# Kernel optimization log

Measured on AMD Instinct MI355X. Metric: run time of the kernel, lower is better.

Reference implementation:

```python
import jax, jax.numpy as jnp
import numpy as np
from jax import lax

D = 1024
N_EXP = 8
DD = 4 * D
BS = 8192
TRAIN_CAP = 1.0
LN_EPS = 1e-5


def setup_inputs() -> dict:
    key = jax.random.key(0)
    ks = jax.random.split(key, 8)
    s = 0.02
    return {
        "x": jax.random.normal(ks[0], (BS, D), jnp.float32),
        "Wg": jax.random.normal(ks[1], (N_EXP, D), jnp.float32) * s,
        "cp_w1": jax.random.normal(ks[2], (D, D), jnp.float32) * s,
        "cp_b1": jnp.zeros((D,), jnp.float32),
        "cp_w2": jax.random.normal(ks[3], (N_EXP, D), jnp.float32) * s,
        "cp_b2": jnp.zeros((N_EXP,), jnp.float32),
        "ln_g": jnp.ones((D,), jnp.float32),
        "ln_b": jnp.zeros((D,), jnp.float32),
        "fc1s": jax.random.normal(ks[4], (N_EXP, DD, D), jnp.float32) * s,
        "b1s": jnp.zeros((N_EXP, DD), jnp.float32),
        "fc2s": jax.random.normal(ks[5], (N_EXP, D, DD), jnp.float32) * s,
        "b2s": jnp.zeros((N_EXP, D), jnp.float32),
    }


def reference(x, Wg, cp_w1, cp_b1, cp_w2, cp_b2, ln_g, ln_b, fc1s, b1s, fc2s, b2s):
    bs, d = x.shape
    n = Wg.shape[0]
    k = int(bs * TRAIN_CAP) // n  # tokens kept per expert

    # gate scores in (0,1): (tanh(x Wg^T)+1)/2   -> [bs, n]
    scores = (jnp.tanh(x @ Wg.T) + 1.0) * 0.5

    # per-expert descending sort of tokens by score
    order = jnp.argsort(-scores, axis=0)                      # [bs, n]
    sorted_w = jnp.take_along_axis(scores, order, axis=0)     # [bs, n]
    kept_w = sorted_w[:k]                                     # [k, n]
    kept_idx = order[:k]                                      # [k, n]

    # keep mask (labels for capacity predictor)
    keep_mask = jnp.zeros((bs, n), x.dtype).at[kept_idx, jnp.arange(n)[None, :]].set(1.0)

    # capacity predictor loss (BCE with logits, x detached)
    xd = lax.stop_gradient(x)
    h = jax.nn.gelu(xd @ cp_w1.T + cp_b1, approximate=True)
    logits = h @ cp_w2.T + cp_b2                              # [bs, n]
    cap_loss = jnp.mean(jnp.logaddexp(0.0, logits) - logits * keep_mask)

    # dispatch: gather selected tokens, row-major flatten of [k, n]
    idx = kept_idx.reshape(-1)                                # [k*n]
    y = x[idx]                                                # [k*n, d]

    # LayerNorm
    mu = y.mean(-1, keepdims=True)
    var = y.var(-1, keepdims=True)
    y = (y - mu) * lax.rsqrt(var + LN_EPS) * ln_g + ln_b

    # per-expert grouped GEMMs
    y3 = y.reshape(k, n, d)
    h1 = jnp.einsum('knd,nfd->knf', y3, fc1s) + b1s[None]     # [k, n, dd]
    h1 = jax.nn.gelu(h1, approximate=True)
    y2 = jnp.einsum('knf,ndf->knd', h1, fc2s) + b2s[None]     # [k, n, d]

    # weight by gate score and scatter-add back (residual)
    y2 = y2 * kept_w[..., None]
    out = x.at[idx].add(y2.reshape(k * n, d))
    return out, cap_loss
```

## Files before the change

kernel.cpp:

```cpp
#include <hip/hip_runtime.h>


#define BS_   8192
#define D_    1024
#define DD_   4096
#define NEXP  8
#define KCAP  1024

typedef unsigned int   uint32;
typedef unsigned short u16;
typedef __bf16 bf16x8  __attribute__((ext_vector_type(8)));
typedef float  f32x4   __attribute__((ext_vector_type(4)));
typedef u16    u16x8   __attribute__((ext_vector_type(8)));
typedef u16    u16x4   __attribute__((ext_vector_type(4)));

__device__ __forceinline__ u16 f2bf(float f){
  uint32 u = __float_as_uint(f);
  u = (u + 0x7fffu + ((u >> 16) & 1u)) >> 16;
  return (u16)u;
}
__device__ __forceinline__ float bf_lo(uint32 u){ return __uint_as_float(u << 16); }
__device__ __forceinline__ float bf_hi(uint32 u){ return __uint_as_float(u & 0xffff0000u); }

__device__ __forceinline__ float gelu_fast(float v){
  const float u2 = v * (1.5957691216057308f + 0.07135481282962162f * v * v);
  const float e  = __expf(u2);
  return v - v / (1.0f + e);
}
__device__ __forceinline__ void glds16(const u16* g, u16* l){
  __builtin_amdgcn_global_load_lds(
      (const __attribute__((address_space(1))) unsigned int*)g,
      (__attribute__((address_space(3))) unsigned int*)l, 16, 0, 0);
}

__global__ __launch_bounds__(256)
void convert_kernel(const float* __restrict__ in, u16* __restrict__ out, int n)
{
  const int stride = gridDim.x * 256 * 8;
  for (int idx = (blockIdx.x * 256 + threadIdx.x) * 8; idx < n; idx += stride){
    const float4 a = *(const float4*)(in + idx);
    const float4 b = *(const float4*)(in + idx + 4);
    u16x8 o;
    o[0]=f2bf(a.x); o[1]=f2bf(a.y); o[2]=f2bf(a.z); o[3]=f2bf(a.w);
    o[4]=f2bf(b.x); o[5]=f2bf(b.y); o[6]=f2bf(b.z); o[7]=f2bf(b.w);
    *(u16x8*)(out + idx) = o;
  }
}

__global__ __launch_bounds__(64)
void gating_kernel(const float* __restrict__ x, const float* __restrict__ Wg,
                   float* __restrict__ scores, uint32* __restrict__ keep_bits,
                   u16* __restrict__ xh)
{
  const int i    = blockIdx.x;
  const int lane = threadIdx.x;
  const float* xr = x + (size_t)i * D_ + lane * 16;
  const float4 x0 = *(const float4*)(xr +  0);
  const float4 x1 = *(const float4*)(xr +  4);
  const float4 x2 = *(const float4*)(xr +  8);
  const float4 x3 = *(const float4*)(xr + 12);
  u16x8 p0, p1;
  p0[0]=f2bf(x0.x); p0[1]=f2bf(x0.y); p0[2]=f2bf(x0.z); p0[3]=f2bf(x0.w);
  p0[4]=f2bf(x1.x); p0[5]=f2bf(x1.y); p0[6]=f2bf(x1.z); p0[7]=f2bf(x1.w);
  p1[0]=f2bf(x2.x); p1[1]=f2bf(x2.y); p1[2]=f2bf(x2.z); p1[3]=f2bf(x2.w);
  p1[4]=f2bf(x3.x); p1[5]=f2bf(x3.y); p1[6]=f2bf(x3.z); p1[7]=f2bf(x3.w);
  *(u16x8*)(xh + (size_t)i * D_ + lane * 16)     = p0;
  *(u16x8*)(xh + (size_t)i * D_ + lane * 16 + 8) = p1;

  float acc[NEXP];
  #pragma unroll
  for (int e = 0; e < NEXP; e++){
    const float* wr = Wg + e * D_ + lane * 16;
    const float4 w0 = *(const float4*)(wr +  0);
    const float4 w1 = *(const float4*)(wr +  4);
    const float4 w2 = *(const float4*)(wr +  8);
    const float4 w3 = *(const float4*)(wr + 12);
    float s = x0.x*w0.x + x0.y*w0.y + x0.z*w0.z + x0.w*w0.w;
    s += x1.x*w1.x + x1.y*w1.y + x1.z*w1.z + x1.w*w1.w;
    s += x2.x*w2.x + x2.y*w2.y + x2.z*w2.z + x2.w*w2.w;
    s += x3.x*w3.x + x3.y*w3.y + x3.z*w3.z + x3.w*w3.w;
    acc[e] = s;
  }
  #pragma unroll
  for (int e = 0; e < NEXP; e++){
    #pragma unroll
    for (int off = 32; off >= 1; off >>= 1) acc[e] += __shfl_xor(acc[e], off);
  }
  if (lane == 0){
    #pragma unroll
    for (int e = 0; e < NEXP; e++) scores[i * NEXP + e] = (tanhf(acc[e]) + 1.0f) * 0.5f;
    keep_bits[i] = 0u;
  }
}

__global__ __launch_bounds__(256)
void select_kernel(const float* __restrict__ scores, uint32* __restrict__ keep_bits,
                   int* __restrict__ counts, int* __restrict__ rowlist,
                   float* __restrict__ wlist, int* __restrict__ inv)
{
  __shared__ unsigned long long sk[2048];
  const int e = blockIdx.y;
  const int i = blockIdx.x * 256 + threadIdx.x;
  const float ms = scores[i * NEXP + e];
  const unsigned long long mk =
      ((unsigned long long)__float_as_uint(ms) << 32) | (uint32)(BS_ - 1 - i);
  int cnt = 0;
  for (int base = 0; base < BS_; base += 2048){
    #pragma unroll
    for (int u = 0; u < 8; u++){
      const int j = base + (int)threadIdx.x * 8 + u;
      const float sj = scores[j * NEXP + e];
      sk[threadIdx.x * 8 + u] =
          ((unsigned long long)__float_as_uint(sj) << 32) | (uint32)(BS_ - 1 - j);
    }
    __syncthreads();
    #pragma unroll 8
    for (int jj = 0; jj < 2048; jj++) cnt += (sk[jj] > mk) ? 1 : 0;
    __syncthreads();
  }
  if (cnt < KCAP){
    const int slot = atomicAdd(&counts[e], 1);
    rowlist[e * KCAP + slot] = i;
    wlist[e * KCAP + slot]   = ms;
    inv[i * NEXP + e]        = slot;
    atomicOr(&keep_bits[i], 1u << e);
  }
}

template<bool GELU_EP, bool OUT_BF16>
__global__ __launch_bounds__(256)
void gemm_bt16(const u16* __restrict__ A, const u16* __restrict__ B,
               const float* __restrict__ bias, void* __restrict__ Cv,
               int M, int N, int K,
               long long sA, long long sB, long long sBias, long long sC)
{
  __shared__ u16 smA[128 * 32];
  __shared__ u16 smB[128 * 32];
  const int z    = blockIdx.z;
  const int m0   = blockIdx.y * 128;
  const int n0   = blockIdx.x * 128;
  const int tid  = threadIdx.x;
  const int lane = tid & 63, wv = tid >> 6;
  const int l15  = lane & 15, quad = lane >> 4;
  const int moff = (wv >> 1) * 64, noff = (wv & 1) * 64;

  const int srow = wv * 32 + (lane >> 2);
  const int skol = (lane & 3) * 8;
  const u16* Ag = A + (long long)z * sA + (long long)(m0 + srow) * K + skol;
  const u16* Bg = B + (long long)z * sB + (long long)(n0 + srow) * K + skol;
  u16* lA = smA + wv * 1024;
  u16* lB = smB + wv * 1024;

  f32x4 acc[4][4];
  #pragma unroll
  for (int i = 0; i < 4; i++)
    #pragma unroll
    for (int j = 0; j < 4; j++)
      acc[i][j] = (f32x4){0.f, 0.f, 0.f, 0.f};

  for (int k0 = 0; k0 < K; k0 += 32){
    #pragma unroll
    for (int c = 0; c < 2; c++){
      glds16(Ag + (long long)(c * 16) * K + k0, lA + c * 512);
      glds16(Bg + (long long)(c * 16) * K + k0, lB + c * 512);
    }
    __syncthreads();
    bf16x8 aF[4], bF[4];
    #pragma unroll
    for (int i = 0; i < 4; i++)
      aF[i] = *(const bf16x8*)(smA + (moff + i * 16 + l15) * 32 + quad * 8);
    #pragma unroll
    for (int j = 0; j < 4; j++)
      bF[j] = *(const bf16x8*)(smB + (noff + j * 16 + l15) * 32 + quad * 8);
    #pragma unroll
    for (int i = 0; i < 4; i++)
      #pragma unroll
      for (int j = 0; j < 4; j++)
        acc[i][j] = __builtin_amdgcn_mfma_f32_16x16x32_bf16(bF[j], aF[i], acc[i][j], 0, 0, 0);
    __syncthreads();
  }

  const float* biasp = bias + (long long)z * sBias;
  const long long cbase = (long long)z * sC;
  #pragma unroll
  for (int i = 0; i < 4; i++){
    const int gm = m0 + moff + i * 16 + l15;
    const long long rowb = cbase + (long long)gm * N;
    #pragma unroll
    for (int j = 0; j < 4; j++){
      const int gn = n0 + noff + j * 16 + quad * 4;
      const float4 bv = *(const float4*)(biasp + gn);
      float v0 = acc[i][j][0] + bv.x;
      float v1 = acc[i][j][1] + bv.y;
      float v2 = acc[i][j][2] + bv.z;
      float v3 = acc[i][j][3] + bv.w;
      if constexpr (GELU_EP){
        v0 = gelu_fast(v0); v1 = gelu_fast(v1);
        v2 = gelu_fast(v2); v3 = gelu_fast(v3);
      }
      if constexpr (OUT_BF16){
        u16x4 o; o[0]=f2bf(v0); o[1]=f2bf(v1); o[2]=f2bf(v2); o[3]=f2bf(v3);
        *(u16x4*)((u16*)Cv + rowb + gn) = o;
      } else {
        *(float4*)((float*)Cv + rowb + gn) = make_float4(v0, v1, v2, v3);
      }
    }
  }
}

__global__ __launch_bounds__(256)
void loss_kernel(const u16* __restrict__ h, const float* __restrict__ cp_w2,
                 const float* __restrict__ cp_b2, const uint32* __restrict__ keep_bits,
                 float* __restrict__ loss)
{
  __shared__ float bl;
  if (threadIdx.x == 0) bl = 0.f;
  __syncthreads();
  const int wv = threadIdx.x >> 6, lane = threadIdx.x & 63;
  const int i  = blockIdx.x * 4 + wv;
  const u16* hr = h + (size_t)i * D_ + lane * 16;
  const uint4 ha = *(const uint4*)(hr);
  const uint4 hb = *(const uint4*)(hr + 8);
  float hx[16];
  hx[0]=bf_lo(ha.x); hx[1]=bf_hi(ha.x); hx[2]=bf_lo(ha.y); hx[3]=bf_hi(ha.y);
  hx[4]=bf_lo(ha.z); hx[5]=bf_hi(ha.z); hx[6]=bf_lo(ha.w); hx[7]=bf_hi(ha.w);
  hx[8]=bf_lo(hb.x); hx[9]=bf_hi(hb.x); hx[10]=bf_lo(hb.y); hx[11]=bf_hi(hb.y);
  hx[12]=bf_lo(hb.z); hx[13]=bf_hi(hb.z); hx[14]=bf_lo(hb.w); hx[15]=bf_hi(hb.w);
  float acc[NEXP];
  #pragma unroll
  for (int e = 0; e < NEXP; e++){
    const float* wr = cp_w2 + e * D_ + lane * 16;
    const float4 w0 = *(const float4*)(wr +  0);
    const float4 w1 = *(const float4*)(wr +  4);
    const float4 w2 = *(const float4*)(wr +  8);
    const float4 w3 = *(const float4*)(wr + 12);
    float s = hx[0]*w0.x + hx[1]*w0.y + hx[2]*w0.z + hx[3]*w0.w;
    s += hx[4]*w1.x + hx[5]*w1.y + hx[6]*w1.z + hx[7]*w1.w;
    s += hx[8]*w2.x + hx[9]*w2.y + hx[10]*w2.z + hx[11]*w2.w;
    s += hx[12]*w3.x + hx[13]*w3.y + hx[14]*w3.z + hx[15]*w3.w;
    acc[e] = s;
  }
  #pragma unroll
  for (int e = 0; e < NEXP; e++){
    #pragma unroll
    for (int off = 32; off >= 1; off >>= 1) acc[e] += __shfl_xor(acc[e], off);
  }
  if (lane == 0){
    const uint32 kb = keep_bits[i];
    float li = 0.f;
    #pragma unroll
    for (int e = 0; e < NEXP; e++){
      const float l  = acc[e] + cp_b2[e];
      const float sp = fmaxf(l, 0.f) + log1pf(expf(-fabsf(l)));
      li += sp - l * (float)((kb >> e) & 1u);
    }
    atomicAdd(&bl, li);
  }
  __syncthreads();
  if (threadIdx.x == 0) atomicAdd(loss, bl);
}

__global__ __launch_bounds__(256)
void ln_gather_kernel(const float* __restrict__ x, const int* __restrict__ rowlist,
                      const float* __restrict__ ln_g, const float* __restrict__ ln_b,
                      u16* __restrict__ Y)
{
  __shared__ float red[8];
  const int b   = blockIdx.x;
  const int row = rowlist[b];
  const int tid = threadIdx.x;
  const float4 v = *(const float4*)(x + (size_t)row * D_ + tid * 4);
  float s = v.x + v.y + v.z + v.w;
  float q = v.x*v.x + v.y*v.y + v.z*v.z + v.w*v.w;
  const int lane = tid & 63, wv = tid >> 6;
  #pragma unroll
  for (int off = 32; off >= 1; off >>= 1){ s += __shfl_xor(s, off); q += __shfl_xor(q, off); }
  if (lane == 0){ red[wv] = s; red[4 + wv] = q; }
  __syncthreads();
  s = red[0] + red[1] + red[2] + red[3];
  q = red[4] + red[5] + red[6] + red[7];
  const float mu  = s * (1.0f / D_);
  const float var = q * (1.0f / D_) - mu * mu;
  const float rs  = rsqrtf(var + 1e-5f);
  const float4 g  = *(const float4*)(ln_g + tid * 4);
  const float4 bb = *(const float4*)(ln_b + tid * 4);
  u16x4 o;
  o[0] = f2bf((v.x - mu) * rs * g.x + bb.x);
  o[1] = f2bf((v.y - mu) * rs * g.y + bb.y);
  o[2] = f2bf((v.z - mu) * rs * g.z + bb.z);
  o[3] = f2bf((v.w - mu) * rs * g.w + bb.w);
  *(u16x4*)(&Y[(size_t)b * D_ + tid * 4]) = o;
}

__global__ __launch_bounds__(256)
void combine_kernel(const float* __restrict__ x, const uint32* __restrict__ keep_bits,
                    const int* __restrict__ inv, const float* __restrict__ wlist,
                    const float* __restrict__ Y2, float* __restrict__ out)
{
  const int i = blockIdx.x;
  const int c = threadIdx.x * 4;
  float4 v = *(const float4*)(x + (size_t)i * D_ + c);
  uint32 kb = keep_bits[i];
  while (kb){
    const int e = __ffs(kb) - 1;
    kb &= kb - 1;
    const int r = inv[i * NEXP + e];
    const float w = wlist[e * KCAP + r];
    const float4 y = *(const float4*)(Y2 + ((size_t)(e * KCAP + r)) * D_ + c);
    v.x += w * y.x; v.y += w * y.y; v.z += w * y.z; v.w += w * y.w;
  }
  *(float4*)(out + (size_t)i * D_ + c) = v;
}

__global__ void finalize_loss_kernel(const float* __restrict__ loss, float* __restrict__ outp){
  outp[0] = loss[0] * (1.0f / (float)(BS_ * NEXP));
}

extern "C" void kernel_launch(void* const* d_in, const int* in_sizes, int n_in,
                              void* d_out, int out_size, void* d_ws, size_t ws_size,
                              hipStream_t stream)
{
  const float* x     = (const float*)d_in[0];
  const float* Wg    = (const float*)d_in[1];
  const float* cp_w1 = (const float*)d_in[2];
  const float* cp_b1 = (const float*)d_in[3];
  const float* cp_w2 = (const float*)d_in[4];
  const float* cp_b2 = (const float*)d_in[5];
  const float* ln_g  = (const float*)d_in[6];
  const float* ln_b  = (const float*)d_in[7];
  const float* fc1s  = (const float*)d_in[8];
  const float* b1s   = (const float*)d_in[9];
  const float* fc2s  = (const float*)d_in[10];
  const float* b2s   = (const float*)d_in[11];
  float* out = (float*)d_out;

  char* p = (char*)d_ws;
  auto take = [&](size_t bytes) -> char* {
    char* r = p; p += (bytes + 255) & ~(size_t)255; return r;
  };
  float*  scores    = (float*) take((size_t)BS_ * NEXP * 4);
  int*    counts    = (int*)   take(256);
  float*  loss      = (float*) take(256);
  int*    rowlist   = (int*)   take((size_t)BS_ * 4);
  float*  wlist     = (float*) take((size_t)BS_ * 4);
  uint32* keep_bits = (uint32*)take((size_t)BS_ * 4);
  int*    inv       = (int*)   take((size_t)BS_ * NEXP * 4);
  u16*    xh        = (u16*)   take((size_t)BS_ * D_ * 2);
  u16*    cpw1h     = (u16*)   take((size_t)D_ * D_ * 2);
  u16*    fc1h      = (u16*)   take((size_t)NEXP * DD_ * D_ * 2);
  u16*    fc2h      = (u16*)   take((size_t)NEXP * D_ * DD_ * 2);
  u16*    H1        = (u16*)   take((size_t)NEXP * KCAP * DD_ * 2);
  u16*    h_cp      = (u16*)   take((size_t)BS_ * D_ * 2);
  u16*    Y         = (u16*)   take((size_t)NEXP * KCAP * D_ * 2);
  float*  Y2        = (float*)h_cp;

  hipMemsetAsync(counts, 0, 512, stream);

  convert_kernel<<<512,  256, 0, stream>>>(cp_w1, cpw1h, D_ * D_);
  convert_kernel<<<8192, 256, 0, stream>>>(fc1s, fc1h, NEXP * DD_ * D_);
  convert_kernel<<<8192, 256, 0, stream>>>(fc2s, fc2h, NEXP * D_ * DD_);

  gating_kernel<<<BS_, 64, 0, stream>>>(x, Wg, scores, keep_bits, xh);

  select_kernel<<<dim3(BS_ / 256, NEXP), 256, 0, stream>>>(
      scores, keep_bits, counts, rowlist, wlist, inv);

  gemm_bt16<true, true><<<dim3(D_ / 128, BS_ / 128, 1), 256, 0, stream>>>(
      xh, cpw1h, cp_b1, h_cp, BS_, D_, D_, 0, 0, 0, 0);

  loss_kernel<<<BS_ / 4, 256, 0, stream>>>(h_cp, cp_w2, cp_b2, keep_bits, loss);

  ln_gather_kernel<<<BS_, 256, 0, stream>>>(x, rowlist, ln_g, ln_b, Y);

  gemm_bt16<true, true><<<dim3(DD_ / 128, KCAP / 128, NEXP), 256, 0, stream>>>(
      Y, fc1h, b1s, H1, KCAP, DD_, D_,
      (long long)KCAP * D_, (long long)DD_ * D_, DD_, (long long)KCAP * DD_);

  gemm_bt16<false, false><<<dim3(D_ / 128, KCAP / 128, NEXP), 256, 0, stream>>>(
      H1, fc2h, b2s, Y2, KCAP, D_, DD_,
      (long long)KCAP * DD_, (long long)D_ * DD_, D_, (long long)KCAP * D_);

  combine_kernel<<<BS_, 256, 0, stream>>>(x, keep_bits, inv, wlist, Y2, out);

  finalize_loss_kernel<<<1, 1, 0, stream>>>(loss, out + (size_t)BS_ * D_);
}
```

Before: 881.4 us.

## Pre-pack B weights into MFMA fragment order, load B from registers, split-K fc2

Weight conversion now writes the B operands in MFMA fragment order, so each lane loads its bf16x8 B fragment straight from global memory into registers, prefetched one K step ahead, instead of staging B through shared memory. This halves LDS traffic and footprint per block. The fc2 GEMM is also split two ways along K into two fp32 partial buffers, which doubles the grid. Bias is added in the combine kernel while it sums the partials. The cost is more global traffic for the partials and a B fragment layout that depends on K being a multiple of 32.

```diff
diff --git a/kernel.cpp b/kernel.cpp
--- a/kernel.cpp
+++ b/kernel.cpp
@@ -34,17 +34,22 @@
 }
 
 __global__ __launch_bounds__(256)
-void convert_kernel(const float* __restrict__ in, u16* __restrict__ out, int n)
-{
-  const int stride = gridDim.x * 256 * 8;
-  for (int idx = (blockIdx.x * 256 + threadIdx.x) * 8; idx < n; idx += stride){
-    const float4 a = *(const float4*)(in + idx);
-    const float4 b = *(const float4*)(in + idx + 4);
-    u16x8 o;
-    o[0]=f2bf(a.x); o[1]=f2bf(a.y); o[2]=f2bf(a.z); o[3]=f2bf(a.w);
-    o[4]=f2bf(b.x); o[5]=f2bf(b.y); o[6]=f2bf(b.z); o[7]=f2bf(b.w);
-    *(u16x8*)(out + idx) = o;
-  }
+void pack_b_kernel(const float* __restrict__ in, u16* __restrict__ out,
+                   int K, int kshift)
+{
+  const long long t = (long long)blockIdx.x * 256 + threadIdx.x;
+  const int  lane  = (int)(t & 63);
+  const long long brick = t >> 6;
+  const long long n16 = brick >> kshift;
+  const int  k32  = (int)(brick & ((1 << kshift) - 1));
+  const float* src = in + (n16 * 16 + (lane & 15)) * (long long)K
+                        + k32 * 32 + (lane >> 4) * 8;
+  const float4 a = *(const float4*)src;
+  const float4 b = *(const float4*)(src + 4);
+  u16x8 o;
+  o[0]=f2bf(a.x); o[1]=f2bf(a.y); o[2]=f2bf(a.z); o[3]=f2bf(a.w);
+  o[4]=f2bf(b.x); o[5]=f2bf(b.y); o[6]=f2bf(b.z); o[7]=f2bf(b.w);
+  *(u16x8*)(out + t * 8) = o;
 }
 
 __global__ __launch_bounds__(64)
@@ -127,16 +132,19 @@
   }
 }
 
-template<bool GELU_EP, bool OUT_BF16>
-__global__ __launch_bounds__(256)
-void gemm_bt16(const u16* __restrict__ A, const u16* __restrict__ B,
-               const float* __restrict__ bias, void* __restrict__ Cv,
-               int M, int N, int K,
-               long long sA, long long sB, long long sBias, long long sC)
+template<bool GELU_EP, bool OUT_BF16, int SPLIT>
+__global__ __launch_bounds__(256)
+void gemm_pk(const u16* __restrict__ A, const u16* __restrict__ Bp,
+             const float* __restrict__ bias, void* __restrict__ Cv,
+             float* __restrict__ P0, float* __restrict__ P1,
+             int M, int N, int K,
+             long long sA, long long sBp, long long sBias, long long sC)
 {
   __shared__ u16 smA[128 * 32];
-  __shared__ u16 smB[128 * 32];
-  const int z    = blockIdx.z;
+  const int zr   = blockIdx.z;
+  const int z    = zr / SPLIT, ks = zr % SPLIT;
+  const int kb0  = (K / SPLIT) * ks;
+  const int kIt0 = kb0 >> 5, kIt1 = (kb0 + K / SPLIT) >> 5;
   const int m0   = blockIdx.y * 128;
   const int n0   = blockIdx.x * 128;
   const int tid  = threadIdx.x;
@@ -147,9 +155,12 @@
   const int srow = wv * 32 + (lane >> 2);
   const int skol = (lane & 3) * 8;
   const u16* Ag = A + (long long)z * sA + (long long)(m0 + srow) * K + skol;
-  const u16* Bg = B + (long long)z * sB + (long long)(n0 + srow) * K + skol;
   u16* lA = smA + wv * 1024;
-  u16* lB = smB + wv * 1024;
+
+  const int nk32 = K >> 5;
+  const long long jstr = (long long)nk32 * 512;
+  const u16* Bfrag = Bp + (long long)z * sBp
+                   + ((long long)((n0 + noff) >> 4)) * jstr + (long long)lane * 8;
 
   f32x4 acc[4][4];
   #pragma unroll
@@ -158,51 +169,74 @@
     for (int j = 0; j < 4; j++)
       acc[i][j] = (f32x4){0.f, 0.f, 0.f, 0.f};
 
-  for (int k0 = 0; k0 < K; k0 += 32){
-    #pragma unroll
-    for (int c = 0; c < 2; c++){
-      glds16(Ag + (long long)(c * 16) * K + k0, lA + c * 512);
-      glds16(Bg + (long long)(c * 16) * K + k0, lB + c * 512);
-    }
+  bf16x8 bF[4], bN[4];
+  #pragma unroll
+  for (int j = 0; j < 4; j++)
+    bF[j] = *(const bf16x8*)(Bfrag + j * jstr + (long long)kIt0 * 512);
+
+  for (int kk = kIt0; kk < kIt1; kk++){
+    glds16(Ag + kk * 32,           lA);
+    glds16(Ag + 16 * K + kk * 32,  lA + 512);
     __syncthreads();
-    bf16x8 aF[4], bF[4];
+    const bool more = (kk + 1 < kIt1);
+    if (more){
+      #pragma unroll
+      for (int j = 0; j < 4; j++)
+        bN[j] = *(const bf16x8*)(Bfrag + j * jstr + (long long)(kk + 1) * 512);
+    }
+    bf16x8 aF[4];
     #pragma unroll
     for (int i = 0; i < 4; i++)
       aF[i] = *(const bf16x8*)(smA + (moff + i * 16 + l15) * 32 + quad * 8);
-    #pragma unroll
-    for (int j = 0; j < 4; j++)
-      bF[j] = *(const bf16x8*)(smB + (noff + j * 16 + l15) * 32 + quad * 8);
     #pragma unroll
     for (int i = 0; i < 4; i++)
       #pragma unroll
       for (int j = 0; j < 4; j++)
         acc[i][j] = __builtin_amdgcn_mfma_f32_16x16x32_bf16(bF[j], aF[i], acc[i][j], 0, 0, 0);
     __syncthreads();
-  }
-
-  const float* biasp = bias + (long long)z * sBias;
-  const long long cbase = (long long)z * sC;
-  #pragma unroll
-  for (int i = 0; i < 4; i++){
-    const int gm = m0 + moff + i * 16 + l15;
-    const long long rowb = cbase + (long long)gm * N;
-    #pragma unroll
-    for (int j = 0; j < 4; j++){
-      const int gn = n0 + noff + j * 16 + quad * 4;
-      const float4 bv = *(const float4*)(biasp + gn);
-      float v0 = acc[i][j][0] + bv.x;
-      float v1 = acc[i][j][1] + bv.y;
-      float v2 = acc[i][j][2] + bv.z;
-      float v3 = acc[i][j][3] + bv.w;
-      if constexpr (GELU_EP){
-        v0 = gelu_fast(v0); v1 = gelu_fast(v1);
-        v2 = gelu_fast(v2); v3 = gelu_fast(v3);
+    if (more){
+      #pragma unroll
+      for (int j = 0; j < 4; j++) bF[j] = bN[j];
+    }
+  }
+
+  if constexpr (SPLIT > 1){
+    float* Pout = (ks == 0 ? P0 : P1) + (long long)z * sC;
+    #pragma unroll
+    for (int i = 0; i < 4; i++){
+      const int gm = m0 + moff + i * 16 + l15;
+      #pragma unroll
+      for (int j = 0; j < 4; j++){
+        const int gn = n0 + noff + j * 16 + quad * 4;
+        *(float4*)(Pout + (long long)gm * N + gn) =
+            make_float4(acc[i][j][0], acc[i][j][1], acc[i][j][2], acc[i][j][3]);
       }
-      if constexpr (OUT_BF16){
-        u16x4 o; o[0]=f2bf(v0); o[1]=f2bf(v1); o[2]=f2bf(v2); o[3]=f2bf(v3);
-        *(u16x4*)((u16*)Cv + rowb + gn) = o;
-      } else {
-        *(float4*)((float*)Cv + rowb + gn) = make_float4(v0, v1, v2, v3);
+    }
+  } else {
+    const float* biasp = bias + (long long)z * sBias;
+    const long long cbase = (long long)z * sC;
+    #pragma unroll
+    for (int i = 0; i < 4; i++){
+      const int gm = m0 + moff + i * 16 + l15;
+      const long long rowb = cbase + (long long)gm * N;
+      #pragma unroll
+      for (int j = 0; j < 4; j++){
+        const int gn = n0 + noff + j * 16 + quad * 4;
+        const float4 bv = *(const float4*)(biasp + gn);
+        float v0 = acc[i][j][0] + bv.x;
+        float v1 = acc[i][j][1] + bv.y;
+        float v2 = acc[i][j][2] + bv.z;
+        float v3 = acc[i][j][3] + bv.w;
+        if constexpr (GELU_EP){
+          v0 = gelu_fast(v0); v1 = gelu_fast(v1);
+          v2 = gelu_fast(v2); v3 = gelu_fast(v3);
+        }
+        if constexpr (OUT_BF16){
+          u16x4 o; o[0]=f2bf(v0); o[1]=f2bf(v1); o[2]=f2bf(v2); o[3]=f2bf(v3);
+          *(u16x4*)((u16*)Cv + rowb + gn) = o;
+        } else {
+          *(float4*)((float*)Cv + rowb + gn) = make_float4(v0, v1, v2, v3);
+        }
       }
     }
   }
@@ -295,7 +329,8 @@
 __global__ __launch_bounds__(256)
 void combine_kernel(const float* __restrict__ x, const uint32* __restrict__ keep_bits,
                     const int* __restrict__ inv, const float* __restrict__ wlist,
-                    const float* __restrict__ Y2, float* __restrict__ out)
+                    const float* __restrict__ P0, const float* __restrict__ P1,
+                    const float* __restrict__ b2s, float* __restrict__ out)
 {
   const int i = blockIdx.x;
   const int c = threadIdx.x * 4;
@@ -306,8 +341,14 @@
     kb &= kb - 1;
     const int r = inv[i * NEXP + e];
     const float w = wlist[e * KCAP + r];
-    const float4 y = *(const float4*)(Y2 + ((size_t)(e * KCAP + r)) * D_ + c);
-    v.x += w * y.x; v.y += w * y.y; v.z += w * y.z; v.w += w * y.w;
+    const size_t ro = ((size_t)(e * KCAP + r)) * D_ + c;
+    const float4 p0 = *(const float4*)(P0 + ro);
+    const float4 p1 = *(const float4*)(P1 + ro);
+    const float4 b2 = *(const float4*)(b2s + (size_t)e * D_ + c);
+    v.x += w * (p0.x + p1.x + b2.x);
+    v.y += w * (p0.y + p1.y + b2.y);
+    v.z += w * (p0.z + p1.z + b2.z);
+    v.w += w * (p0.w + p1.w + b2.w);
   }
   *(float4*)(out + (size_t)i * D_ + c) = v;
 }
@@ -346,41 +387,42 @@
   uint32* keep_bits = (uint32*)take((size_t)BS_ * 4);
   int*    inv       = (int*)   take((size_t)BS_ * NEXP * 4);
   u16*    xh        = (u16*)   take((size_t)BS_ * D_ * 2);
-  u16*    cpw1h     = (u16*)   take((size_t)D_ * D_ * 2);
-  u16*    fc1h      = (u16*)   take((size_t)NEXP * DD_ * D_ * 2);
-  u16*    fc2h      = (u16*)   take((size_t)NEXP * D_ * DD_ * 2);
+  u16*    cpw1p     = (u16*)   take((size_t)D_ * D_ * 2);
+  u16*    fc1p      = (u16*)   take((size_t)NEXP * DD_ * D_ * 2);
+  u16*    fc2p      = (u16*)   take((size_t)NEXP * D_ * DD_ * 2);
   u16*    H1        = (u16*)   take((size_t)NEXP * KCAP * DD_ * 2);
   u16*    h_cp      = (u16*)   take((size_t)BS_ * D_ * 2);
   u16*    Y         = (u16*)   take((size_t)NEXP * KCAP * D_ * 2);
-  float*  Y2        = (float*)h_cp;
+  float*  Pt0       = (float*)xh;
+  float*  Pt1       = (float*)((char*)xh + ((size_t)32 << 20));
 
   hipMemsetAsync(counts, 0, 512, stream);
 
-  convert_kernel<<<512,  256, 0, stream>>>(cp_w1, cpw1h, D_ * D_);
-  convert_kernel<<<8192, 256, 0, stream>>>(fc1s, fc1h, NEXP * DD_ * D_);
-  convert_kernel<<<8192, 256, 0, stream>>>(fc2s, fc2h, NEXP * D_ * DD_);
+  pack_b_kernel<<<(D_ * D_ / 8) / 256, 256, 0, stream>>>(cp_w1, cpw1p, D_, 5);
+  pack_b_kernel<<<(NEXP * DD_ * D_ / 8) / 256, 256, 0, stream>>>(fc1s, fc1p, D_, 5);
+  pack_b_kernel<<<(NEXP * D_ * DD_ / 8) / 256, 256, 0, stream>>>(fc2s, fc2p, DD_, 7);
 
   gating_kernel<<<BS_, 64, 0, stream>>>(x, Wg, scores, keep_bits, xh);
 
   select_kernel<<<dim3(BS_ / 256, NEXP), 256, 0, stream>>>(
       scores, keep_bits, counts, rowlist, wlist, inv);
 
-  gemm_bt16<true, true><<<dim3(D_ / 128, BS_ / 128, 1), 256, 0, stream>>>(
-      xh, cpw1h, cp_b1, h_cp, BS_, D_, D_, 0, 0, 0, 0);
+  gemm_pk<true, true, 1><<<dim3(D_ / 128, BS_ / 128, 1), 256, 0, stream>>>(
+      xh, cpw1p, cp_b1, h_cp, nullptr, nullptr, BS_, D_, D_, 0, 0, 0, 0);
 
   loss_kernel<<<BS_ / 4, 256, 0, stream>>>(h_cp, cp_w2, cp_b2, keep_bits, loss);
 
   ln_gather_kernel<<<BS_, 256, 0, stream>>>(x, rowlist, ln_g, ln_b, Y);
 
-  gemm_bt16<true, true><<<dim3(DD_ / 128, KCAP / 128, NEXP), 256, 0, stream>>>(
-      Y, fc1h, b1s, H1, KCAP, DD_, D_,
+  gemm_pk<true, true, 1><<<dim3(DD_ / 128, KCAP / 128, NEXP), 256, 0, stream>>>(
+      Y, fc1p, b1s, H1, nullptr, nullptr, KCAP, DD_, D_,
       (long long)KCAP * D_, (long long)DD_ * D_, DD_, (long long)KCAP * DD_);
 
-  gemm_bt16<false, false><<<dim3(D_ / 128, KCAP / 128, NEXP), 256, 0, stream>>>(
-      H1, fc2h, b2s, Y2, KCAP, D_, DD_,
-      (long long)KCAP * DD_, (long long)D_ * DD_, D_, (long long)KCAP * D_);
-
-  combine_kernel<<<BS_, 256, 0, stream>>>(x, keep_bits, inv, wlist, Y2, out);
+  gemm_pk<false, false, 2><<<dim3(D_ / 128, KCAP / 128, NEXP * 2), 256, 0, stream>>>(
+      H1, fc2p, nullptr, nullptr, Pt0, Pt1, KCAP, D_, DD_,
+      (long long)KCAP * DD_, (long long)D_ * DD_, 0, (long long)KCAP * D_);
+
+  combine_kernel<<<BS_, 256, 0, stream>>>(x, keep_bits, inv, wlist, Pt0, Pt1, b2s, out);
 
   finalize_loss_kernel<<<1, 1, 0, stream>>>(loss, out + (size_t)BS_ * D_);
 }
```

Measured after the change: 851.4 us. 1.04x faster.
